# Performance work log

Measured on AMD Instinct MI355X. Metric: run time of the kernel, lower is better.

The kernel has to match this reference:

```python
import jax, jax.numpy as jnp
import numpy as np

EPS = 1e-5
NHEAD = 8

def layer_norm(x, g, b):
    mu = jnp.mean(x, axis=-1, keepdims=True)
    var = jnp.mean((x - mu) ** 2, axis=-1, keepdims=True)
    return (x - mu) * jax.lax.rsqrt(var + EPS) * g + b

def setup_inputs() -> dict:
    key = jax.random.key(0)
    ks = jax.random.split(key, 8)
    B, S, D, F = 4, 2048, 512, 2048
    s = 0.02
    return {
        "x": jax.random.normal(ks[0], (B, S, D), jnp.float32),
        "Wqkv": jax.random.normal(ks[1], (3 * D, D), jnp.float32) * s,
        "bqkv": jnp.zeros((3 * D,), jnp.float32),
        "Wo": jax.random.normal(ks[2], (D, D), jnp.float32) * s,
        "bo": jnp.zeros((D,), jnp.float32),
        "W1": jax.random.normal(ks[3], (F, D), jnp.float32) * s,
        "b1": jnp.zeros((F,), jnp.float32),
        "W2": jax.random.normal(ks[4], (D, F), jnp.float32) * s,
        "b2": jnp.zeros((D,), jnp.float32),
        "g1": jnp.ones((D,), jnp.float32),
        "bn1": jnp.zeros((D,), jnp.float32),
        "g2": jnp.ones((D,), jnp.float32),
        "bn2": jnp.zeros((D,), jnp.float32),
    }

def reference(x, Wqkv, bqkv, Wo, bo, W1, b1, W2, b2, g1, bn1, g2, bn2):
    B, S, D = x.shape
    H = NHEAD
    hd = D // H
    # fused QKV projection (torch MultiheadAttention in_proj)
    qkv = x @ Wqkv.T + bqkv                      # [B,S,3D]
    q, k, v = jnp.split(qkv, 3, axis=-1)
    q = q.reshape(B, S, H, hd).transpose(0, 2, 1, 3)  # [B,H,S,hd]
    k = k.reshape(B, S, H, hd).transpose(0, 2, 1, 3)
    v = v.reshape(B, S, H, hd).transpose(0, 2, 1, 3)
    scores = jnp.einsum("bhqd,bhkd->bhqk", q, k) / jnp.sqrt(jnp.float32(hd))
    causal = jnp.tril(jnp.ones((S, S), bool))
    scores = jnp.where(causal, scores, jnp.float32(-jnp.inf))
    attn = jax.nn.softmax(scores, axis=-1)
    ctx = jnp.einsum("bhqk,bhkd->bhqd", attn, v)        # [B,H,S,hd]
    ctx = ctx.transpose(0, 2, 1, 3).reshape(B, S, D)
    attn_out = ctx @ Wo.T + bo
    # residual + LayerNorm 1
    x = layer_norm(x + attn_out, g1, bn1)
    # FFN (ReLU) + residual + LayerNorm 2
    ff = jax.nn.relu(x @ W1.T + b1) @ W2.T + b2
    x = layer_norm(x + ff, g2, bn2)
    return x
```

## Files before the change

### kernel.cpp

```cpp
#include <hip/hip_runtime.h>
#include <hip/hip_bf16.h>
#include <math.h>

#define D_MODEL 512
#define SEQ     2048
#define BATCH   4
#define NHEADS  8
#define HDIM    64
#define FFN     2048
#define TOKENS  (BATCH*SEQ)

typedef __attribute__((ext_vector_type(8))) short bf16x8;
typedef __attribute__((ext_vector_type(4))) float f32x4;

__device__ inline ushort f2bf(float f) {
    unsigned u = __builtin_bit_cast(unsigned, f);
    unsigned r = (u + 0x7fffu + ((u >> 16) & 1u)) >> 16;
    return (ushort)r;
}
__device__ inline ushort f2bf_fast(float f) {
    return (ushort)((__builtin_bit_cast(unsigned, f) + 0x8000u) >> 16);
}
__device__ inline float bf2f(ushort u) {
    return __builtin_bit_cast(float, (unsigned)u << 16);
}

#define GLOAD_LDS16(g, l) __builtin_amdgcn_global_load_lds( \
    (const __attribute__((address_space(1))) void*)(g), \
    (__attribute__((address_space(3))) void*)(l), 16, 0, 0)

__global__ void cast_all_bf16(const float* __restrict__ x, const float* __restrict__ Wqkv,
                              const float* __restrict__ Wo, const float* __restrict__ W1,
                              const float* __restrict__ W2, ushort* __restrict__ outbase) {
    const int i = blockIdx.x * blockDim.x + threadIdx.x;
    if (i >= 1835008) return;
    float4 v;
    if      (i < 1048576) v = ((const float4*)x)[i];
    else if (i < 1245184) v = ((const float4*)Wqkv)[i - 1048576];
    else if (i < 1310720) v = ((const float4*)Wo)[i - 1245184];
    else if (i < 1572864) v = ((const float4*)W1)[i - 1310720];
    else                  v = ((const float4*)W2)[i - 1572864];
    ushort4 o;
    o.x = f2bf(v.x); o.y = f2bf(v.y); o.z = f2bf(v.z); o.w = f2bf(v.w);
    ((ushort4*)outbase)[i] = o;
}

template<int MODE, int RELU, int RES>
__global__ __launch_bounds__(256) void gemm_bt_mfma(const ushort* __restrict__ A,
                                                    const ushort* __restrict__ W,
                                                    const float* __restrict__ bias,
                                                    void* __restrict__ CoutA,
                                                    void* __restrict__ CoutB,
                                                    const void* __restrict__ Res,
                                                    ushort* __restrict__ Qc,
                                                    ushort* __restrict__ Kc,
                                                    ushort* __restrict__ Vt,
                                                    int M, int N, int Kstride, int Klen) {
    __shared__ ushort Asb[2][128 * 32];
    __shared__ ushort Bsb[2][128 * 32];

    const int tid  = threadIdx.x;
    const int lane = tid & 63;
    const int wv   = tid >> 6;
    const int m0   = blockIdx.y * 128;
    const int n0   = blockIdx.x * 128;
    const int wm   = (wv >> 1) * 64;
    const int wn   = (wv & 1) * 64;
    const int ksel = (MODE == 3) ? blockIdx.z : 0;

    const ushort* Ab = A + (size_t)ksel * Klen;
    const ushort* Wb = W + (size_t)ksel * Klen;

    const int eA = wv * 1024 + lane * 8;
    const int rA = eA >> 5, cA = eA & 31;
    const ushort* gA0 = Ab + (size_t)(m0 + rA) * Kstride + cA;
    const ushort* gA1 = gA0 + (size_t)16 * Kstride;
    const ushort* gB0 = Wb + (size_t)(n0 + rA) * Kstride + cA;
    const ushort* gB1 = gB0 + (size_t)16 * Kstride;
    ushort* lA0 = &Asb[0][wv * 1024];
    ushort* lA1 = &Asb[0][wv * 1024 + 512];
    ushort* lB0 = &Bsb[0][wv * 1024];
    ushort* lB1 = &Bsb[0][wv * 1024 + 512];
    ushort* lA0h = &Asb[1][wv * 1024];
    ushort* lA1h = &Asb[1][wv * 1024 + 512];
    ushort* lB0h = &Bsb[1][wv * 1024];
    ushort* lB1h = &Bsb[1][wv * 1024 + 512];

    f32x4 acc[4][4] = {};

    const int fr = lane & 15;
    const int fk = (lane >> 4) * 8;

    for (int k0 = 0; k0 < Klen; k0 += 64) {
        GLOAD_LDS16(gA0, lA0);  GLOAD_LDS16(gA1, lA1);
        GLOAD_LDS16(gB0, lB0);  GLOAD_LDS16(gB1, lB1);
        GLOAD_LDS16(gA0 + 32, lA0h); GLOAD_LDS16(gA1 + 32, lA1h);
        GLOAD_LDS16(gB0 + 32, lB0h); GLOAD_LDS16(gB1 + 32, lB1h);
        gA0 += 64; gA1 += 64; gB0 += 64; gB1 += 64;
        __syncthreads();

        #pragma unroll
        for (int h = 0; h < 2; ++h) {
            bf16x8 af[4], bfr[4];
            #pragma unroll
            for (int i = 0; i < 4; ++i)
                af[i] = *(const bf16x8*)(&Asb[h][(wm + i * 16 + fr) * 32 + fk]);
            #pragma unroll
            for (int j = 0; j < 4; ++j)
                bfr[j] = *(const bf16x8*)(&Bsb[h][(wn + j * 16 + fr) * 32 + fk]);
            #pragma unroll
            for (int i = 0; i < 4; ++i)
                #pragma unroll
                for (int j = 0; j < 4; ++j)
                    acc[i][j] = __builtin_amdgcn_mfma_f32_16x16x32_bf16(af[i], bfr[j], acc[i][j], 0, 0, 0);
        }
        __syncthreads();
    }

    const int col  = lane & 15;
    const int rowq = (lane >> 4) * 4;
    #pragma unroll
    for (int i = 0; i < 4; ++i) {
        const int gm = m0 + wm + i * 16 + rowq;
        #pragma unroll
        for (int j = 0; j < 4; ++j) {
            const int gn = n0 + wn + j * 16 + col;
            if (MODE == 2) {
                const float bv = bias[gn];
                const int seg = gn >> 9;
                const int h   = (gn >> 6) & 7;
                const int dd  = gn & 63;
                const int bb  = gm >> 11;
                const int ss  = gm & 2047;
                const int bh  = bb * 8 + h;
                if (seg == 2) {
                    ushort4 pk;
                    pk.x = f2bf(acc[i][j][0] + bv);
                    pk.y = f2bf(acc[i][j][1] + bv);
                    pk.z = f2bf(acc[i][j][2] + bv);
                    pk.w = f2bf(acc[i][j][3] + bv);
                    *(ushort4*)(Vt + ((size_t)bh * 64 + dd) * 2048 + ss) = pk;
                } else {
                    ushort* dst = (seg == 0 ? Qc : Kc) + ((size_t)bh * 2048 + ss) * 64 + dd;
                    #pragma unroll
                    for (int r = 0; r < 4; ++r)
                        dst[(size_t)r * 64] = f2bf(acc[i][j][r] + bv);
                }
            } else if (MODE == 3) {
                ushort* dst = (ushort*)(ksel ? CoutB : CoutA);
                #pragma unroll
                for (int r = 0; r < 4; ++r) {
                    float v = acc[i][j][r];
                    if (!ksel) {
                        v += bias[gn];
                        if (RES == 1) v += ((const float*)Res)[(size_t)(gm + r) * N + gn];
                        if (RES == 2) v += bf2f(((const ushort*)Res)[(size_t)(gm + r) * N + gn]);
                    }
                    dst[(size_t)(gm + r) * N + gn] = f2bf(v);
                }
            } else {
                const float bv = bias[gn];
                #pragma unroll
                for (int r = 0; r < 4; ++r) {
                    float v = acc[i][j][r] + bv;
                    if (RELU) v = fmaxf(v, 0.f);
                    ((ushort*)CoutA)[(size_t)(gm + r) * N + gn] = f2bf(v);
                }
            }
        }
    }
}

__device__ __forceinline__ void attn_step(const ushort* __restrict__ Kb,
                                          const ushort* __restrict__ Vb,
                                          ushort* __restrict__ Psw,
                                          bf16x8 qf0, bf16x8 qf1,
                                          float (&lp)[4], f32x4 (&o)[4],
                                          int qw, int j0, bool diag,
                                          int col, int g, int c7) {
    f32x4 s[4] = {};
    #pragma unroll
    for (int nt = 0; nt < 4; ++nt) {
        const int kr = nt * 16 + col;
        bf16x8 kf0 = *(const bf16x8*)(Kb + kr * 64 + (((g    ) ^ c7) * 8));
        bf16x8 kf1 = *(const bf16x8*)(Kb + kr * 64 + (((g + 4) ^ c7) * 8));
        s[nt] = __builtin_amdgcn_mfma_f32_16x16x32_bf16(qf0, kf0, s[nt], 0, 0, 0);
        s[nt] = __builtin_amdgcn_mfma_f32_16x16x32_bf16(qf1, kf1, s[nt], 0, 0, 0);
    }

    if (diag) {
        #pragma unroll
        for (int nt = 0; nt < 4; ++nt)
            #pragma unroll
            for (int r = 0; r < 4; ++r)
                if ((j0 + nt * 16 + col) > (qw + 4 * g + r)) s[nt][r] = -INFINITY;
    }

    #pragma unroll
    for (int nt = 0; nt < 4; ++nt)
        #pragma unroll
        for (int r = 0; r < 4; ++r) {
            float p = __expf(s[nt][r] * 0.125f);
            s[nt][r] = p;
            lp[r] += p;
        }

    #pragma unroll
    for (int nt = 0; nt < 4; ++nt)
        #pragma unroll
        for (int r = 0; r < 4; ++r) {
            const int q  = 4 * g + r;
            const int bc = 32 * nt + 2 * col;
            *(ushort*)((char*)Psw + q * 128 + (((bc >> 4) ^ (q & 7)) * 16) + (bc & 15)) =
                f2bf_fast(s[nt][r]);
        }

    {
        bf16x8 pf0 = *(const bf16x8*)(Psw + col * 64 + (((g    ) ^ c7) * 8));
        bf16x8 pf1 = *(const bf16x8*)(Psw + col * 64 + (((g + 4) ^ c7) * 8));
        #pragma unroll
        for (int nt = 0; nt < 4; ++nt) {
            const int vr = nt * 16 + col;
            bf16x8 vf0 = *(const bf16x8*)(Vb + vr * 64 + (((g    ) ^ c7) * 8));
            bf16x8 vf1 = *(const bf16x8*)(Vb + vr * 64 + (((g + 4) ^ c7) * 8));
            o[nt] = __builtin_amdgcn_mfma_f32_16x16x32_bf16(pf0, vf0, o[nt], 0, 0, 0);
            o[nt] = __builtin_amdgcn_mfma_f32_16x16x32_bf16(pf1, vf1, o[nt], 0, 0, 0);
        }
    }
}

__global__ __launch_bounds__(256) void attn_mfma_kernel(const ushort* __restrict__ Qc,
                                                        const ushort* __restrict__ Kc,
                                                        const ushort* __restrict__ Vt,
                                                        ushort* __restrict__ ctxb) {
    __shared__ ushort Ks[2 * 64 * 64];
    __shared__ ushort Vs[2 * 64 * 64];
    __shared__ ushort Ps[64 * 64];

    const int tid  = threadIdx.x;
    const int lane = tid & 63;
    const int wv   = tid >> 6;
    const int pair = blockIdx.x;
    const int bh   = blockIdx.y;
    const int q0a  = pair * 64;
    const int q0b  = (31 - pair) * 64;
    const int qwA  = q0a + wv * 16;
    const int qwB  = q0b + wv * 16;

    const int col = lane & 15;
    const int g   = lane >> 4;
    const int c7  = col & 7;

    bf16x8 qfA0, qfA1, qfB0, qfB1;
    {
        const ushort* qa = Qc + ((size_t)bh * 2048 + qwA + col) * 64 + g * 8;
        qfA0 = *(const bf16x8*)qa;
        qfA1 = *(const bf16x8*)(qa + 32);
        const ushort* qb = Qc + ((size_t)bh * 2048 + qwB + col) * 64 + g * 8;
        qfB0 = *(const bf16x8*)qb;
        qfB1 = *(const bf16x8*)(qb + 32);
    }

    const int srow = tid >> 2;
    const int sch  = 2 * (tid & 3);
    const ushort* Kg = Kc + ((size_t)bh * 2048 + srow) * 64 + sch * 8;
    const ushort* Vg = Vt + ((size_t)bh * 64 + srow) * 2048 + sch * 8;
    const int ko0 = srow * 64 + (((sch    ) ^ (srow & 7)) * 8);
    const int ko1 = srow * 64 + (((sch + 1) ^ (srow & 7)) * 8);
    ushort* Psw = Ps + wv * 1024;

    float lpa[4] = {}, lpb[4] = {};
    f32x4 oa[4] = {}, ob[4] = {};

    bf16x8 pk0 = *(const bf16x8*)(Kg);
    bf16x8 pk1 = *(const bf16x8*)(Kg + 8);
    bf16x8 pv0 = *(const bf16x8*)(Vg);
    bf16x8 pv1 = *(const bf16x8*)(Vg + 8);

    for (int j0 = 0; j0 <= q0b; j0 += 64) {
        const int par = (j0 >> 6) & 1;
        ushort* Kb = Ks + par * 4096;
        ushort* Vb = Vs + par * 4096;
        *(bf16x8*)(Kb + ko0) = pk0; *(bf16x8*)(Kb + ko1) = pk1;
        *(bf16x8*)(Vb + ko0) = pv0; *(bf16x8*)(Vb + ko1) = pv1;
        __syncthreads();

        if (j0 < q0b) {
            pk0 = *(const bf16x8*)(Kg + (size_t)(j0 + 64) * 64);
            pk1 = *(const bf16x8*)(Kg + (size_t)(j0 + 64) * 64 + 8);
            pv0 = *(const bf16x8*)(Vg + j0 + 64);
            pv1 = *(const bf16x8*)(Vg + j0 + 72);
        }

        if (j0 <= q0a)
            attn_step(Kb, Vb, Psw, qfA0, qfA1, lpa, oa, qwA, j0, j0 == q0a, col, g, c7);
        attn_step(Kb, Vb, Psw, qfB0, qfB1, lpb, ob, qwB, j0, j0 == q0b, col, g, c7);
    }

    const int b = bh >> 3, h = bh & 7;
    #pragma unroll
    for (int r = 0; r < 4; ++r) {
        float la = lpa[r];
        la += __shfl_xor(la, 1); la += __shfl_xor(la, 2);
        la += __shfl_xor(la, 4); la += __shfl_xor(la, 8);
        float lb = lpb[r];
        lb += __shfl_xor(lb, 1); lb += __shfl_xor(lb, 2);
        lb += __shfl_xor(lb, 4); lb += __shfl_xor(lb, 8);
        const float inva = 1.f / la;
        const float invb = 1.f / lb;
        const size_t rowa = ((size_t)b * 2048 + qwA + 4 * g + r) * 512 + h * 64;
        const size_t rowb = ((size_t)b * 2048 + qwB + 4 * g + r) * 512 + h * 64;
        #pragma unroll
        for (int nt = 0; nt < 4; ++nt) {
            ctxb[rowa + nt * 16 + col] = f2bf(oa[nt][r] * inva);
            ctxb[rowb + nt * 16 + col] = f2bf(ob[nt][r] * invb);
        }
    }
}

template<int OUTMODE>
__global__ void ln_residual2(const ushort* __restrict__ B1, const ushort* __restrict__ B2,
                             const float* __restrict__ g, const float* __restrict__ beta,
                             float* __restrict__ out, ushort* __restrict__ outb) {
    __shared__ float sbuf[8];
    const int row = blockIdx.x;
    const int tid = threadIdx.x;
    const size_t base = (size_t)row * D_MODEL;

    ushort2 p1 = ((const ushort2*)(B1 + base))[tid];
    ushort2 p2 = ((const ushort2*)(B2 + base))[tid];
    float v0 = bf2f(p1.x) + bf2f(p2.x);
    float v1 = bf2f(p1.y) + bf2f(p2.y);

    float sum = v0 + v1;
    #pragma unroll
    for (int off = 32; off; off >>= 1) sum += __shfl_xor(sum, off);
    if ((tid & 63) == 0) sbuf[tid >> 6] = sum;
    __syncthreads();
    if (tid == 0) { float t = 0.f; for (int i = 0; i < 4; ++i) t += sbuf[i]; sbuf[4] = t; }
    __syncthreads();
    const float mu = sbuf[4] * (1.f / 512.f);
    __syncthreads();

    float d0 = v0 - mu, d1 = v1 - mu;
    float sq = d0 * d0 + d1 * d1;
    #pragma unroll
    for (int off = 32; off; off >>= 1) sq += __shfl_xor(sq, off);
    if ((tid & 63) == 0) sbuf[tid >> 6] = sq;
    __syncthreads();
    if (tid == 0) { float t = 0.f; for (int i = 0; i < 4; ++i) t += sbuf[i]; sbuf[4] = t; }
    __syncthreads();
    const float var = sbuf[4] * (1.f / 512.f);
    const float rs  = rsqrtf(var + 1e-5f);

    float2 gv = ((const float2*)g)[tid];
    float2 bv = ((const float2*)beta)[tid];
    float r0 = d0 * rs * gv.x + bv.x;
    float r1 = d1 * rs * gv.y + bv.y;
    if (OUTMODE == 0) {
        float2 o2; o2.x = r0; o2.y = r1;
        ((float2*)(out + base))[tid] = o2;
    } else {
        ushort2 o2; o2.x = f2bf(r0); o2.y = f2bf(r1);
        ((ushort2*)(outb + base))[tid] = o2;
    }
}

extern "C" void kernel_launch(void* const* d_in, const int* in_sizes, int n_in,
                              void* d_out, int out_size, void* d_ws, size_t ws_size,
                              hipStream_t stream) {
    const float* x    = (const float*)d_in[0];
    const float* Wqkv = (const float*)d_in[1];
    const float* bqkv = (const float*)d_in[2];
    const float* Wo   = (const float*)d_in[3];
    const float* bo   = (const float*)d_in[4];
    const float* W1   = (const float*)d_in[5];
    const float* b1   = (const float*)d_in[6];
    const float* W2   = (const float*)d_in[7];
    const float* b2   = (const float*)d_in[8];
    const float* g1   = (const float*)d_in[9];
    const float* bn1  = (const float*)d_in[10];
    const float* g2   = (const float*)d_in[11];
    const float* bn2  = (const float*)d_in[12];

    float* ws = (float*)d_ws;
    ushort* Qcb    = (ushort*)ws;
    ushort* Kcb    = (ushort*)(ws + 2097152);
    ushort* Vtb    = (ushort*)(ws + 4194304);
    ushort* ff1b   = (ushort*)ws;
    ushort* attn_a = (ushort*)(ws + 8388608);
    ushort* attn_b = (ushort*)(ws + 10485760);
    ushort* ff2a   = (ushort*)(ws + 12582912);
    ushort* ff2b   = (ushort*)(ws + 14680064);
    ushort* ln1b   = (ushort*)(ws + 16777216);
    ushort* ctxb   = (ushort*)(ws + 20971520);
    ushort* xb     = (ushort*)(ws + 25165824);
    ushort* Wqkvb  = (ushort*)(ws + 27262976);
    ushort* Wob    = (ushort*)(ws + 27656192);
    ushort* W1b    = (ushort*)(ws + 27787264);
    ushort* W2b    = (ushort*)(ws + 28311552);
    float*  out    = (float*)d_out;

    const dim3 blk(256);

    cast_all_bf16<<<dim3(7168), blk, 0, stream>>>(x, Wqkv, Wo, W1, W2, xb);

    gemm_bt_mfma<2,0,0><<<dim3(12, 64), blk, 0, stream>>>(
        xb, Wqkvb, bqkv, nullptr, nullptr, nullptr, Qcb, Kcb, Vtb, TOKENS, 1536, 512, 512);
    attn_mfma_kernel<<<dim3(16, BATCH*NHEADS), blk, 0, stream>>>(Qcb, Kcb, Vtb, ctxb);
    gemm_bt_mfma<3,0,1><<<dim3(4, 64, 2), blk, 0, stream>>>(
        ctxb, Wob, bo, attn_a, attn_b, x, nullptr, nullptr, nullptr, TOKENS, 512, 512, 256);
    ln_residual2<1><<<dim3(TOKENS), blk, 0, stream>>>(attn_a, attn_b, g1, bn1, nullptr, ln1b);
    gemm_bt_mfma<1,1,0><<<dim3(16, 64), blk, 0, stream>>>(
        ln1b, W1b, b1, ff1b, nullptr, nullptr, nullptr, nullptr, nullptr, TOKENS, 2048, 512, 512);
    gemm_bt_mfma<3,0,2><<<dim3(4, 64, 2), blk, 0, stream>>>(
        ff1b, W2b, b2, ff2a, ff2b, ln1b, nullptr, nullptr, nullptr, TOKENS, 512, 2048, 1024);
    ln_residual2<0><<<dim3(TOKENS), blk, 0, stream>>>(ff2a, ff2b, g2, bn2, out, nullptr);
}
```

Before: 271.6 us.

## Split attention KV loop across two wave groups and shrink GEMM K-tile

```diff
diff --git a/kernel.cpp b/kernel.cpp
--- a/kernel.cpp
+++ b/kernel.cpp
@@ -24,6 +24,8 @@
 __device__ inline float bf2f(ushort u) {
     return __builtin_bit_cast(float, (unsigned)u << 16);
 }
+
+#define EXP_C 0.18033688011112042f
 
 #define GLOAD_LDS16(g, l) __builtin_amdgcn_global_load_lds( \
     (const __attribute__((address_space(1))) void*)(g), \
@@ -56,8 +58,8 @@
                                                     ushort* __restrict__ Kc,
                                                     ushort* __restrict__ Vt,
                                                     int M, int N, int Kstride, int Klen) {
-    __shared__ ushort Asb[2][128 * 32];
-    __shared__ ushort Bsb[2][128 * 32];
+    __shared__ ushort Asb[128 * 32];
+    __shared__ ushort Bsb[128 * 32];
 
     const int tid  = threadIdx.x;
     const int lane = tid & 63;
@@ -77,43 +79,35 @@
     const ushort* gA1 = gA0 + (size_t)16 * Kstride;
     const ushort* gB0 = Wb + (size_t)(n0 + rA) * Kstride + cA;
     const ushort* gB1 = gB0 + (size_t)16 * Kstride;
-    ushort* lA0 = &Asb[0][wv * 1024];
-    ushort* lA1 = &Asb[0][wv * 1024 + 512];
-    ushort* lB0 = &Bsb[0][wv * 1024];
-    ushort* lB1 = &Bsb[0][wv * 1024 + 512];
-    ushort* lA0h = &Asb[1][wv * 1024];
-    ushort* lA1h = &Asb[1][wv * 1024 + 512];
-    ushort* lB0h = &Bsb[1][wv * 1024];
-    ushort* lB1h = &Bsb[1][wv * 1024 + 512];
+    ushort* lA0 = Asb + wv * 1024;
+    ushort* lA1 = Asb + wv * 1024 + 512;
+    ushort* lB0 = Bsb + wv * 1024;
+    ushort* lB1 = Bsb + wv * 1024 + 512;
 
     f32x4 acc[4][4] = {};
 
     const int fr = lane & 15;
     const int fk = (lane >> 4) * 8;
 
-    for (int k0 = 0; k0 < Klen; k0 += 64) {
-        GLOAD_LDS16(gA0, lA0);  GLOAD_LDS16(gA1, lA1);
-        GLOAD_LDS16(gB0, lB0);  GLOAD_LDS16(gB1, lB1);
-        GLOAD_LDS16(gA0 + 32, lA0h); GLOAD_LDS16(gA1 + 32, lA1h);
-        GLOAD_LDS16(gB0 + 32, lB0h); GLOAD_LDS16(gB1 + 32, lB1h);
-        gA0 += 64; gA1 += 64; gB0 += 64; gB1 += 64;
+    for (int k0 = 0; k0 < Klen; k0 += 32) {
+        GLOAD_LDS16(gA0, lA0); GLOAD_LDS16(gA1, lA1);
+        GLOAD_LDS16(gB0, lB0); GLOAD_LDS16(gB1, lB1);
+        gA0 += 32; gA1 += 32; gB0 += 32; gB1 += 32;
         __syncthreads();
 
-        #pragma unroll
-        for (int h = 0; h < 2; ++h) {
-            bf16x8 af[4], bfr[4];
-            #pragma unroll
-            for (int i = 0; i < 4; ++i)
-                af[i] = *(const bf16x8*)(&Asb[h][(wm + i * 16 + fr) * 32 + fk]);
+        bf16x8 af[4], bfr[4];
+        #pragma unroll
+        for (int i = 0; i < 4; ++i)
+            af[i] = *(const bf16x8*)(Asb + (wm + i * 16 + fr) * 32 + fk);
+        #pragma unroll
+        for (int j = 0; j < 4; ++j)
+            bfr[j] = *(const bf16x8*)(Bsb + (wn + j * 16 + fr) * 32 + fk);
+
+        #pragma unroll
+        for (int i = 0; i < 4; ++i)
             #pragma unroll
             for (int j = 0; j < 4; ++j)
-                bfr[j] = *(const bf16x8*)(&Bsb[h][(wn + j * 16 + fr) * 32 + fk]);
-            #pragma unroll
-            for (int i = 0; i < 4; ++i)
-                #pragma unroll
-                for (int j = 0; j < 4; ++j)
-                    acc[i][j] = __builtin_amdgcn_mfma_f32_16x16x32_bf16(af[i], bfr[j], acc[i][j], 0, 0, 0);
-        }
+                acc[i][j] = __builtin_amdgcn_mfma_f32_16x16x32_bf16(af[i], bfr[j], acc[i][j], 0, 0, 0);
         __syncthreads();
     }
 
@@ -200,7 +194,7 @@
     for (int nt = 0; nt < 4; ++nt)
         #pragma unroll
         for (int r = 0; r < 4; ++r) {
-            float p = __expf(s[nt][r] * 0.125f);
+            float p = exp2f(s[nt][r] * EXP_C);
             s[nt][r] = p;
             lp[r] += p;
         }
@@ -229,27 +223,31 @@
     }
 }
 
-__global__ __launch_bounds__(256) void attn_mfma_kernel(const ushort* __restrict__ Qc,
+__global__ __launch_bounds__(512) void attn_mfma_kernel(const ushort* __restrict__ Qc,
                                                         const ushort* __restrict__ Kc,
                                                         const ushort* __restrict__ Vt,
                                                         ushort* __restrict__ ctxb) {
-    __shared__ ushort Ks[2 * 64 * 64];
-    __shared__ ushort Vs[2 * 64 * 64];
-    __shared__ ushort Ps[64 * 64];
+    __shared__ __align__(16) char smem[49152];
 
     const int tid  = threadIdx.x;
     const int lane = tid & 63;
     const int wv   = tid >> 6;
+    const int gr   = wv >> 2;
+    const int qsub = wv & 3;
     const int pair = blockIdx.x;
     const int bh   = blockIdx.y;
     const int q0a  = pair * 64;
     const int q0b  = (31 - pair) * 64;
-    const int qwA  = q0a + wv * 16;
-    const int qwB  = q0b + wv * 16;
+    const int qwA  = q0a + qsub * 16;
+    const int qwB  = q0b + qsub * 16;
 
     const int col = lane & 15;
     const int g   = lane >> 4;
     const int c7  = col & 7;
+
+    ushort* Kb  = (ushort*)(smem + gr * 16384);
+    ushort* Vb  = (ushort*)(smem + gr * 16384 + 8192);
+    ushort* Psw = (ushort*)(smem + 32768 + wv * 2048);
 
     bf16x8 qfA0, qfA1, qfB0, qfB1;
     {
@@ -261,59 +259,95 @@
         qfB1 = *(const bf16x8*)(qb + 32);
     }
 
-    const int srow = tid >> 2;
-    const int sch  = 2 * (tid & 3);
+    const int lt   = tid & 255;
+    const int srow = lt >> 2;
+    const int sch  = 2 * (lt & 3);
     const ushort* Kg = Kc + ((size_t)bh * 2048 + srow) * 64 + sch * 8;
     const ushort* Vg = Vt + ((size_t)bh * 64 + srow) * 2048 + sch * 8;
     const int ko0 = srow * 64 + (((sch    ) ^ (srow & 7)) * 8);
     const int ko1 = srow * 64 + (((sch + 1) ^ (srow & 7)) * 8);
-    ushort* Psw = Ps + wv * 1024;
+
+    const int maxidx = 31 - pair;
+    const int T = (maxidx >> 1) + 1;
 
     float lpa[4] = {}, lpb[4] = {};
     f32x4 oa[4] = {}, ob[4] = {};
 
-    bf16x8 pk0 = *(const bf16x8*)(Kg);
-    bf16x8 pk1 = *(const bf16x8*)(Kg + 8);
-    bf16x8 pv0 = *(const bf16x8*)(Vg);
-    bf16x8 pv1 = *(const bf16x8*)(Vg + 8);
-
-    for (int j0 = 0; j0 <= q0b; j0 += 64) {
-        const int par = (j0 >> 6) & 1;
-        ushort* Kb = Ks + par * 4096;
-        ushort* Vb = Vs + par * 4096;
-        *(bf16x8*)(Kb + ko0) = pk0; *(bf16x8*)(Kb + ko1) = pk1;
-        *(bf16x8*)(Vb + ko0) = pv0; *(bf16x8*)(Vb + ko1) = pv1;
+    bf16x8 pk0 = *(const bf16x8*)(Kg + (size_t)(gr * 64) * 64);
+    bf16x8 pk1 = *(const bf16x8*)(Kg + (size_t)(gr * 64) * 64 + 8);
+    bf16x8 pv0 = *(const bf16x8*)(Vg + gr * 64);
+    bf16x8 pv1 = *(const bf16x8*)(Vg + gr * 64 + 8);
+
+    for (int t = 0; t < T; ++t) {
+        const int idx   = 2 * t + gr;
+        const int j0    = idx * 64;
+        const bool valid = idx <= maxidx;
+        if (valid) {
+            *(bf16x8*)(Kb + ko0) = pk0; *(bf16x8*)(Kb + ko1) = pk1;
+            *(bf16x8*)(Vb + ko0) = pv0; *(bf16x8*)(Vb + ko1) = pv1;
+        }
         __syncthreads();
 
-        if (j0 < q0b) {
-            pk0 = *(const bf16x8*)(Kg + (size_t)(j0 + 64) * 64);
-            pk1 = *(const bf16x8*)(Kg + (size_t)(j0 + 64) * 64 + 8);
-            pv0 = *(const bf16x8*)(Vg + j0 + 64);
-            pv1 = *(const bf16x8*)(Vg + j0 + 72);
-        }
-
-        if (j0 <= q0a)
-            attn_step(Kb, Vb, Psw, qfA0, qfA1, lpa, oa, qwA, j0, j0 == q0a, col, g, c7);
-        attn_step(Kb, Vb, Psw, qfB0, qfB1, lpb, ob, qwB, j0, j0 == q0b, col, g, c7);
-    }
-
-    const int b = bh >> 3, h = bh & 7;
-    #pragma unroll
-    for (int r = 0; r < 4; ++r) {
-        float la = lpa[r];
-        la += __shfl_xor(la, 1); la += __shfl_xor(la, 2);
-        la += __shfl_xor(la, 4); la += __shfl_xor(la, 8);
-        float lb = lpb[r];
-        lb += __shfl_xor(lb, 1); lb += __shfl_xor(lb, 2);
-        lb += __shfl_xor(lb, 4); lb += __shfl_xor(lb, 8);
-        const float inva = 1.f / la;
-        const float invb = 1.f / lb;
-        const size_t rowa = ((size_t)b * 2048 + qwA + 4 * g + r) * 512 + h * 64;
-        const size_t rowb = ((size_t)b * 2048 + qwB + 4 * g + r) * 512 + h * 64;
-        #pragma unroll
-        for (int nt = 0; nt < 4; ++nt) {
-            ctxb[rowa + nt * 16 + col] = f2bf(oa[nt][r] * inva);
-            ctxb[rowb + nt * 16 + col] = f2bf(ob[nt][r] * invb);
+        const int nidx = idx + 2;
+        if (nidx <= maxidx) {
+            pk0 = *(const bf16x8*)(Kg + (size_t)(nidx * 64) * 64);
+            pk1 = *(const bf16x8*)(Kg + (size_t)(nidx * 64) * 64 + 8);
+            pv0 = *(const bf16x8*)(Vg + nidx * 64);
+            pv1 = *(const bf16x8*)(Vg + nidx * 64 + 8);
+        }
+
+        if (valid) {
+            if (idx <= pair)
+                attn_step(Kb, Vb, Psw, qfA0, qfA1, lpa, oa, qwA, j0, idx == pair, col, g, c7);
+            attn_step(Kb, Vb, Psw, qfB0, qfB1, lpb, ob, qwB, j0, idx == maxidx, col, g, c7);
+        }
+        __syncthreads();
+    }
+
+    float* cmb = (float*)smem;
+    if (gr == 1) {
+        float* d = cmb + (wv - 4) * 2560 + lane * 40;
+        #pragma unroll
+        for (int nt = 0; nt < 4; ++nt)
+            #pragma unroll
+            for (int r = 0; r < 4; ++r) {
+                d[nt * 4 + r]      = oa[nt][r];
+                d[16 + nt * 4 + r] = ob[nt][r];
+            }
+        #pragma unroll
+        for (int r = 0; r < 4; ++r) { d[32 + r] = lpa[r]; d[36 + r] = lpb[r]; }
+    }
+    __syncthreads();
+    if (gr == 0) {
+        const float* sP = cmb + wv * 2560 + lane * 40;
+        #pragma unroll
+        for (int nt = 0; nt < 4; ++nt)
+            #pragma unroll
+            for (int r = 0; r < 4; ++r) {
+                oa[nt][r] += sP[nt * 4 + r];
+                ob[nt][r] += sP[16 + nt * 4 + r];
+            }
+        #pragma unroll
+        for (int r = 0; r < 4; ++r) { lpa[r] += sP[32 + r]; lpb[r] += sP[36 + r]; }
+
+        const int b = bh >> 3, h = bh & 7;
+        #pragma unroll
+        for (int r = 0; r < 4; ++r) {
+            float la = lpa[r];
+            la += __shfl_xor(la, 1); la += __shfl_xor(la, 2);
+            la += __shfl_xor(la, 4); la += __shfl_xor(la, 8);
+            float lb = lpb[r];
+            lb += __shfl_xor(lb, 1); lb += __shfl_xor(lb, 2);
+            lb += __shfl_xor(lb, 4); lb += __shfl_xor(lb, 8);
+            const float inva = 1.f / la;
+            const float invb = 1.f / lb;
+            const size_t rowa = ((size_t)b * 2048 + qwA + 4 * g + r) * 512 + h * 64;
+            const size_t rowb = ((size_t)b * 2048 + qwB + 4 * g + r) * 512 + h * 64;
+            #pragma unroll
+            for (int nt = 0; nt < 4; ++nt) {
+                ctxb[rowa + nt * 16 + col] = f2bf(oa[nt][r] * inva);
+                ctxb[rowb + nt * 16 + col] = f2bf(ob[nt][r] * invb);
+            }
         }
     }
 }
@@ -407,7 +441,7 @@
 
     gemm_bt_mfma<2,0,0><<<dim3(12, 64), blk, 0, stream>>>(
         xb, Wqkvb, bqkv, nullptr, nullptr, nullptr, Qcb, Kcb, Vtb, TOKENS, 1536, 512, 512);
-    attn_mfma_kernel<<<dim3(16, BATCH*NHEADS), blk, 0, stream>>>(Qcb, Kcb, Vtb, ctxb);
+    attn_mfma_kernel<<<dim3(16, BATCH*NHEADS), dim3(512), 0, stream>>>(Qcb, Kcb, Vtb, ctxb);
     gemm_bt_mfma<3,0,1><<<dim3(4, 64, 2), blk, 0, stream>>>(
         ctxb, Wob, bo, attn_a, attn_b, x, nullptr, nullptr, nullptr, TOKENS, 512, 512, 256);
     ln_residual2<1><<<dim3(TOKENS), blk, 0, stream>>>(attn_a, attn_b, g1, bn1, nullptr, ln1b);
```

After: 291.0 us. 1.07x slower.

## Halve GEMM K-step, use exp2 in softmax, one-wave-per-row LayerNorm

Applied to the files above, without the earlier changes.

```diff
diff --git a/kernel.cpp b/kernel.cpp
--- a/kernel.cpp
+++ b/kernel.cpp
@@ -24,6 +24,8 @@
 __device__ inline float bf2f(ushort u) {
     return __builtin_bit_cast(float, (unsigned)u << 16);
 }
+
+#define EXP_C 0.18033688011112042f
 
 #define GLOAD_LDS16(g, l) __builtin_amdgcn_global_load_lds( \
     (const __attribute__((address_space(1))) void*)(g), \
@@ -56,8 +58,8 @@
                                                     ushort* __restrict__ Kc,
                                                     ushort* __restrict__ Vt,
                                                     int M, int N, int Kstride, int Klen) {
-    __shared__ ushort Asb[2][128 * 32];
-    __shared__ ushort Bsb[2][128 * 32];
+    __shared__ ushort Asb[128 * 32];
+    __shared__ ushort Bsb[128 * 32];
 
     const int tid  = threadIdx.x;
     const int lane = tid & 63;
@@ -77,43 +79,35 @@
     const ushort* gA1 = gA0 + (size_t)16 * Kstride;
     const ushort* gB0 = Wb + (size_t)(n0 + rA) * Kstride + cA;
     const ushort* gB1 = gB0 + (size_t)16 * Kstride;
-    ushort* lA0 = &Asb[0][wv * 1024];
-    ushort* lA1 = &Asb[0][wv * 1024 + 512];
-    ushort* lB0 = &Bsb[0][wv * 1024];
-    ushort* lB1 = &Bsb[0][wv * 1024 + 512];
-    ushort* lA0h = &Asb[1][wv * 1024];
-    ushort* lA1h = &Asb[1][wv * 1024 + 512];
-    ushort* lB0h = &Bsb[1][wv * 1024];
-    ushort* lB1h = &Bsb[1][wv * 1024 + 512];
+    ushort* lA0 = Asb + wv * 1024;
+    ushort* lA1 = Asb + wv * 1024 + 512;
+    ushort* lB0 = Bsb + wv * 1024;
+    ushort* lB1 = Bsb + wv * 1024 + 512;
 
     f32x4 acc[4][4] = {};
 
     const int fr = lane & 15;
     const int fk = (lane >> 4) * 8;
 
-    for (int k0 = 0; k0 < Klen; k0 += 64) {
-        GLOAD_LDS16(gA0, lA0);  GLOAD_LDS16(gA1, lA1);
-        GLOAD_LDS16(gB0, lB0);  GLOAD_LDS16(gB1, lB1);
-        GLOAD_LDS16(gA0 + 32, lA0h); GLOAD_LDS16(gA1 + 32, lA1h);
-        GLOAD_LDS16(gB0 + 32, lB0h); GLOAD_LDS16(gB1 + 32, lB1h);
-        gA0 += 64; gA1 += 64; gB0 += 64; gB1 += 64;
+    for (int k0 = 0; k0 < Klen; k0 += 32) {
+        GLOAD_LDS16(gA0, lA0); GLOAD_LDS16(gA1, lA1);
+        GLOAD_LDS16(gB0, lB0); GLOAD_LDS16(gB1, lB1);
+        gA0 += 32; gA1 += 32; gB0 += 32; gB1 += 32;
         __syncthreads();
 
-        #pragma unroll
-        for (int h = 0; h < 2; ++h) {
-            bf16x8 af[4], bfr[4];
-            #pragma unroll
-            for (int i = 0; i < 4; ++i)
-                af[i] = *(const bf16x8*)(&Asb[h][(wm + i * 16 + fr) * 32 + fk]);
+        bf16x8 af[4], bfr[4];
+        #pragma unroll
+        for (int i = 0; i < 4; ++i)
+            af[i] = *(const bf16x8*)(Asb + (wm + i * 16 + fr) * 32 + fk);
+        #pragma unroll
+        for (int j = 0; j < 4; ++j)
+            bfr[j] = *(const bf16x8*)(Bsb + (wn + j * 16 + fr) * 32 + fk);
+
+        #pragma unroll
+        for (int i = 0; i < 4; ++i)
             #pragma unroll
             for (int j = 0; j < 4; ++j)
-                bfr[j] = *(const bf16x8*)(&Bsb[h][(wn + j * 16 + fr) * 32 + fk]);
-            #pragma unroll
-            for (int i = 0; i < 4; ++i)
-                #pragma unroll
-                for (int j = 0; j < 4; ++j)
-                    acc[i][j] = __builtin_amdgcn_mfma_f32_16x16x32_bf16(af[i], bfr[j], acc[i][j], 0, 0, 0);
-        }
+                acc[i][j] = __builtin_amdgcn_mfma_f32_16x16x32_bf16(af[i], bfr[j], acc[i][j], 0, 0, 0);
         __syncthreads();
     }
 
@@ -200,7 +194,7 @@
     for (int nt = 0; nt < 4; ++nt)
         #pragma unroll
         for (int r = 0; r < 4; ++r) {
-            float p = __expf(s[nt][r] * 0.125f);
+            float p = exp2f(s[nt][r] * EXP_C);
             s[nt][r] = p;
             lp[r] += p;
         }
@@ -319,50 +313,58 @@
 }
 
 template<int OUTMODE>
-__global__ void ln_residual2(const ushort* __restrict__ B1, const ushort* __restrict__ B2,
-                             const float* __restrict__ g, const float* __restrict__ beta,
-                             float* __restrict__ out, ushort* __restrict__ outb) {
-    __shared__ float sbuf[8];
-    const int row = blockIdx.x;
-    const int tid = threadIdx.x;
-    const size_t base = (size_t)row * D_MODEL;
-
-    ushort2 p1 = ((const ushort2*)(B1 + base))[tid];
-    ushort2 p2 = ((const ushort2*)(B2 + base))[tid];
-    float v0 = bf2f(p1.x) + bf2f(p2.x);
-    float v1 = bf2f(p1.y) + bf2f(p2.y);
-
-    float sum = v0 + v1;
+__global__ __launch_bounds__(256) void ln_residual2(const ushort* __restrict__ B1,
+                                                    const ushort* __restrict__ B2,
+                                                    const float* __restrict__ g,
+                                                    const float* __restrict__ beta,
+                                                    float* __restrict__ out,
+                                                    ushort* __restrict__ outb) {
+    const int lane = threadIdx.x & 63;
+    const int row  = blockIdx.x * 4 + (threadIdx.x >> 6);
+    const size_t base = (size_t)row * D_MODEL + lane * 8;
+
+    bf16x8 p1 = *(const bf16x8*)(B1 + base);
+    bf16x8 p2 = *(const bf16x8*)(B2 + base);
+    float v[8];
+    float sum = 0.f;
+    #pragma unroll
+    for (int i = 0; i < 8; ++i) {
+        v[i] = bf2f((ushort)p1[i]) + bf2f((ushort)p2[i]);
+        sum += v[i];
+    }
     #pragma unroll
     for (int off = 32; off; off >>= 1) sum += __shfl_xor(sum, off);
-    if ((tid & 63) == 0) sbuf[tid >> 6] = sum;
-    __syncthreads();
-    if (tid == 0) { float t = 0.f; for (int i = 0; i < 4; ++i) t += sbuf[i]; sbuf[4] = t; }
-    __syncthreads();
-    const float mu = sbuf[4] * (1.f / 512.f);
-    __syncthreads();
-
-    float d0 = v0 - mu, d1 = v1 - mu;
-    float sq = d0 * d0 + d1 * d1;
+    const float mu = sum * (1.f / 512.f);
+
+    float sq = 0.f;
+    #pragma unroll
+    for (int i = 0; i < 8; ++i) { v[i] -= mu; sq += v[i] * v[i]; }
     #pragma unroll
     for (int off = 32; off; off >>= 1) sq += __shfl_xor(sq, off);
-    if ((tid & 63) == 0) sbuf[tid >> 6] = sq;
-    __syncthreads();
-    if (tid == 0) { float t = 0.f; for (int i = 0; i < 4; ++i) t += sbuf[i]; sbuf[4] = t; }
-    __syncthreads();
-    const float var = sbuf[4] * (1.f / 512.f);
-    const float rs  = rsqrtf(var + 1e-5f);
-
-    float2 gv = ((const float2*)g)[tid];
-    float2 bv = ((const float2*)beta)[tid];
-    float r0 = d0 * rs * gv.x + bv.x;
-    float r1 = d1 * rs * gv.y + bv.y;
+    const float rs = rsqrtf(sq * (1.f / 512.f) + 1e-5f);
+
+    const float4* gv = (const float4*)(g    + lane * 8);
+    const float4* bv = (const float4*)(beta + lane * 8);
+    float4 g0 = gv[0], g1v = gv[1];
+    float4 b0 = bv[0], b1v = bv[1];
+    float r[8];
+    r[0] = v[0]*rs*g0.x + b0.x;  r[1] = v[1]*rs*g0.y + b0.y;
+    r[2] = v[2]*rs*g0.z + b0.z;  r[3] = v[3]*rs*g0.w + b0.w;
+    r[4] = v[4]*rs*g1v.x + b1v.x; r[5] = v[5]*rs*g1v.y + b1v.y;
+    r[6] = v[6]*rs*g1v.z + b1v.z; r[7] = v[7]*rs*g1v.w + b1v.w;
+
     if (OUTMODE == 0) {
-        float2 o2; o2.x = r0; o2.y = r1;
-        ((float2*)(out + base))[tid] = o2;
+        float4* o4 = (float4*)(out + base);
+        float4 o0, o1;
+        o0.x = r[0]; o0.y = r[1]; o0.z = r[2]; o0.w = r[3];
+        o1.x = r[4]; o1.y = r[5]; o1.z = r[6]; o1.w = r[7];
+        o4[0] = o0; o4[1] = o1;
     } else {
-        ushort2 o2; o2.x = f2bf(r0); o2.y = f2bf(r1);
-        ((ushort2*)(outb + base))[tid] = o2;
+        ushort4 u0, u1;
+        u0.x = f2bf(r[0]); u0.y = f2bf(r[1]); u0.z = f2bf(r[2]); u0.w = f2bf(r[3]);
+        u1.x = f2bf(r[4]); u1.y = f2bf(r[5]); u1.z = f2bf(r[6]); u1.w = f2bf(r[7]);
+        ushort4* o4 = (ushort4*)(outb + base);
+        o4[0] = u0; o4[1] = u1;
     }
 }
 
@@ -410,10 +412,10 @@
     attn_mfma_kernel<<<dim3(16, BATCH*NHEADS), blk, 0, stream>>>(Qcb, Kcb, Vtb, ctxb);
     gemm_bt_mfma<3,0,1><<<dim3(4, 64, 2), blk, 0, stream>>>(
         ctxb, Wob, bo, attn_a, attn_b, x, nullptr, nullptr, nullptr, TOKENS, 512, 512, 256);
-    ln_residual2<1><<<dim3(TOKENS), blk, 0, stream>>>(attn_a, attn_b, g1, bn1, nullptr, ln1b);
+    ln_residual2<1><<<dim3(TOKENS / 4), blk, 0, stream>>>(attn_a, attn_b, g1, bn1, nullptr, ln1b);
     gemm_bt_mfma<1,1,0><<<dim3(16, 64), blk, 0, stream>>>(
         ln1b, W1b, b1, ff1b, nullptr, nullptr, nullptr, nullptr, nullptr, TOKENS, 2048, 512, 512);
     gemm_bt_mfma<3,0,2><<<dim3(4, 64, 2), blk, 0, stream>>>(
         ff1b, W2b, b2, ff2a, ff2b, ln1b, nullptr, nullptr, nullptr, TOKENS, 512, 2048, 1024);
-    ln_residual2<0><<<dim3(TOKENS), blk, 0, stream>>>(ff2a, ff2b, g2, bn2, out, nullptr);
-}
+    ln_residual2<0><<<dim3(TOKENS / 4), blk, 0, stream>>>(ff2a, ff2b, g2, bn2, out, nullptr);
+}
```

After: 284.9 us. +4.9%, slower.
